# Performance work log

Hardware: AMD Instinct MI355X
Metric: run time of the kernel (lower is better)

Reference implementation:

```python
import jax, jax.numpy as jnp
import numpy as np


def _rel_coords_log(ws: int) -> np.ndarray:
    # matches torch.meshgrid default indexing='ij'
    idx = np.arange(ws, dtype=np.float32)
    coords = np.stack(np.meshgrid(idx, idx, indexing='ij'), axis=0).reshape(2, -1)  # [2, ws^2]
    rel = coords[:, :, None] - coords[:, None, :]  # [2, T, T]
    rel = rel.transpose(1, 2, 0).reshape(-1, 2)    # [T*T, 2]
    return np.sign(rel) * np.log1p(np.abs(rel))


def setup_inputs() -> dict:
    key = jax.random.key(0)
    ks = jax.random.split(key, 9)
    B, C, Hd, ws, meta_h = 256, 256, 8, 16, 256
    s = 1.0 / np.sqrt(C)
    return {
        'x': jax.random.normal(ks[0], (B, C, ws, ws), dtype=jnp.float32),
        'w_qkv': jax.random.normal(ks[1], (3 * C, C), dtype=jnp.float32) * s,
        'b_qkv': jax.random.normal(ks[2], (3 * C,), dtype=jnp.float32) * 0.01,
        'w_proj': jax.random.normal(ks[3], (C, C), dtype=jnp.float32) * s,
        'b_proj': jax.random.normal(ks[4], (C,), dtype=jnp.float32) * 0.01,
        'mw1': jax.random.normal(ks[5], (meta_h, 2), dtype=jnp.float32) * 0.5,
        'mb1': jax.random.normal(ks[6], (meta_h,), dtype=jnp.float32) * 0.01,
        'mw2': jax.random.normal(ks[7], (Hd, meta_h), dtype=jnp.float32) * (1.0 / np.sqrt(meta_h)),
        'mb2': jax.random.normal(ks[8], (Hd,), dtype=jnp.float32) * 0.01,
        'tau': jnp.ones((1, Hd, 1, 1), dtype=jnp.float32),
    }


def reference(x, w_qkv, b_qkv, w_proj, b_proj, mw1, mb1, mw2, mb2, tau):
    B, C, H, W = x.shape
    T = H * W
    nh = tau.shape[1]
    hd = C // nh
    # [B, C, H, W] -> [B, T, C]
    xt = x.reshape(B, C, T).transpose(0, 2, 1)
    qkv = xt @ w_qkv.T + b_qkv                                  # [B, T, 3C]
    qkv = qkv.reshape(B, T, 3, nh, hd).transpose(2, 0, 3, 1, 4)  # [3, B, nh, T, hd]
    q, k, v = qkv[0], qkv[1], qkv[2]
    # cosine similarity attention
    qn = jnp.linalg.norm(q, axis=-1, keepdims=True)              # [B, nh, T, 1]
    kn = jnp.linalg.norm(k, axis=-1, keepdims=True)
    denom = jnp.maximum(qn * kn.transpose(0, 1, 3, 2), 1e-6)
    scores = jnp.einsum('bhqd,bhkd->bhqk', q, k) / denom
    scores = scores / jnp.maximum(tau, 0.01)
    # MLP relative position bias (static coords)
    rc = jnp.asarray(_rel_coords_log(H))                          # [T*T, 2]
    bias = jax.nn.relu(rc @ mw1.T + mb1) @ mw2.T + mb2            # [T*T, nh]
    bias = bias.T.reshape(nh, T, T)
    scores = scores + bias[None]
    attn = jax.nn.softmax(scores, axis=-1)
    out = jnp.einsum('bhqk,bhkd->bhqd', attn, v)                  # [B, nh, T, hd]
    out = out.transpose(0, 2, 1, 3).reshape(B, T, C)
    out = out @ w_proj.T + b_proj
    return out.transpose(0, 2, 1).reshape(B, C, H, W)
```

## Files before the change

### kernel.cpp

```cpp
#include <hip/hip_runtime.h>
#include <math.h>

#define Cc 256
#define NH 8
#define HD 32
#define Tt 256
#define MH 256
#define TBL 961

typedef _Float16 f16;
typedef f16 f16x4 __attribute__((ext_vector_type(4)));
typedef f16 f16x8 __attribute__((ext_vector_type(8)));
typedef float f32x4 __attribute__((ext_vector_type(4)));

__device__ __forceinline__ f16x8 ld8(const f16* base, int row, int kc) {
  return *(const f16x8*)&base[row * 32 + ((kc ^ ((row >> 2) & 3)) << 3)];
}
__device__ __forceinline__ void st8(f16* base, int row, int kc, f16x8 v) {
  *(f16x8*)&base[row * 32 + ((kc ^ ((row >> 2) & 3)) << 3)] = v;
}
__device__ __forceinline__ int sidx(int row, int col) {
  return row * 32 + (((col >> 3) ^ ((row >> 2) & 3)) << 3) + (col & 7);
}
__device__ __forceinline__ int vsidx(int d, int t) {
  return d * 256 + (((t >> 3) ^ (d & 7)) << 3) + (t & 7);
}
__device__ __forceinline__ f16x8 vld8(const f16* base, int d, int tch) {
  return *(const f16x8*)&base[d * 256 + ((tch ^ (d & 7)) << 3)];
}

__global__ __launch_bounds__(256) void stage0_kernel(
    const float* __restrict__ x, f16* __restrict__ xt,
    const float* __restrict__ mw1, const float* __restrict__ mb1,
    const float* __restrict__ mw2, const float* __restrict__ mb2,
    const float* __restrict__ w_proj, const float* __restrict__ w_qkv,
    float* __restrict__ table, float* __restrict__ tablemax,
    f16* __restrict__ wpf, f16* __restrict__ wqf) {
  __shared__ __align__(16) char smem0[9216];
  int tid = threadIdx.x;
  int blk = blockIdx.x;

  if (blk < 4096) {
    f16* tile = (f16*)smem0;
    int b = blk >> 4, ti = (blk >> 2) & 3, tj = blk & 3;
    const float* xb = x + (size_t)b * 65536;
    int t4 = (tid & 15) * 4, cg = tid >> 4;
#pragma unroll
    for (int p = 0; p < 4; p++) {
      int cl = cg + p * 16;
      float4 v = *(const float4*)&xb[(size_t)(ti * 64 + cl) * 256 + tj * 64 + t4];
      const float* vp = (const float*)&v;
#pragma unroll
      for (int u = 0; u < 4; u++) {
        int tl = t4 + u;
        tile[tl * 72 + (((cl >> 3) ^ ((tl >> 2) & 7)) << 3) + (cl & 7)] = (f16)vp[u];
      }
    }
    __syncthreads();
    f16* xtb = xt + (size_t)b * 65536;
    int tr = tid >> 3, ck = tid & 7;
#pragma unroll
    for (int u = 0; u < 2; u++) {
      int r = tr + u * 32;
      f16x8 v = *(const f16x8*)&tile[r * 72 + ((ck ^ ((r >> 2) & 7)) << 3)];
      *(f16x8*)&xtb[(size_t)(tj * 64 + r) * 256 + ti * 64 + ck * 8] = v;
    }
    return;
  }

  blk -= 4096;
  if (blk >= NH + 32) {
    int blk2 = blk - NH - 32;
#pragma unroll
    for (int pass = 0; pass < 4; pass++) {
      int chunkid = blk2 * 256 + tid + pass * 6144;
      int row = chunkid >> 5, ck = chunkid & 31;
      int hh = row / 96, n = row % 96;
      int srow = ((n >> 5) << 8) + (hh << 5) + (n & 31);
      const float* wp = w_qkv + (size_t)srow * Cc + ck * 8;
      f16x8 v;
#pragma unroll
      for (int u = 0; u < 8; u++) v[u] = (f16)wp[u];
      *(f16x8*)&wqf[(size_t)row * Cc + ck * 8] = v;
    }
    return;
  }
  if (blk >= NH) {
    int base = (blk - NH) * 2048 + tid * 8;
    f16x8 v;
#pragma unroll
    for (int u = 0; u < 8; u++) v[u] = (f16)w_proj[base + u];
    *(f16x8*)&wpf[base] = v;
    return;
  }
  float4* s_w = (float4*)smem0;
  float* red = (float*)(smem0 + 4096);
  for (int i = tid; i < MH; i += 256) {
    float4 w;
    w.x = mw1[2 * i];
    w.y = mw1[2 * i + 1];
    w.z = mb1[i];
    w.w = mw2[blk * MH + i];
    s_w[i] = w;
  }
  __syncthreads();
  float b2 = mb2[blk];
  float d0v[4], d1v[4], ov[4];
#pragma unroll
  for (int j = 0; j < 4; j++) {
    int idx = tid + j * 256;
    int ii = idx < TBL ? idx : TBL - 1;
    float fdi = (float)(ii / 31 - 15);
    float fdj = (float)(ii % 31 - 15);
    d0v[j] = (fdi > 0.f ? 1.f : (fdi < 0.f ? -1.f : 0.f)) * log1pf(fabsf(fdi));
    d1v[j] = (fdj > 0.f ? 1.f : (fdj < 0.f ? -1.f : 0.f)) * log1pf(fabsf(fdj));
    ov[j] = b2;
  }
  for (int m = 0; m < MH; m++) {
    float4 w = s_w[m];
#pragma unroll
    for (int j = 0; j < 4; j++) {
      float hid = fmaxf(fmaf(d0v[j], w.x, fmaf(d1v[j], w.y, w.z)), 0.f);
      ov[j] = fmaf(hid, w.w, ov[j]);
    }
  }
  float lmax = -1e30f;
#pragma unroll
  for (int j = 0; j < 4; j++) {
    int idx = tid + j * 256;
    if (idx < TBL) {
      table[blk * TBL + idx] = ov[j];
      lmax = fmaxf(lmax, ov[j]);
    }
  }
  red[tid] = lmax;
  __syncthreads();
  for (int s = 128; s > 0; s >>= 1) {
    if (tid < s) red[tid] = fmaxf(red[tid], red[tid + s]);
    __syncthreads();
  }
  if (tid == 0) tablemax[blk] = red[0];
}

__global__ __launch_bounds__(512, 4) void fused_attn(
    const f16* __restrict__ xt, const f16* __restrict__ wqf,
    const float* __restrict__ b_qkv, const float* __restrict__ table,
    const float* __restrict__ tablemax, const float* __restrict__ tau,
    f16* __restrict__ attnH) {
  __shared__ __align__(16) char smem[67328];
  f16* Qa = (f16*)smem;
  f16* Ka = (f16*)(smem + 16384);
  f16* Vt = (f16*)(smem + 32768);
  f16* Pspare = (f16*)(smem + 49152);
  float* tbv = (float*)(smem + 51456);
  f16* Xa = (f16*)smem;
  f16* Wa = (f16*)(smem + 16384);

  int tid = threadIdx.x;
  int o = blockIdx.x;
  int bh = ((o & 7) << 8) | (o >> 3);
  int b = bh >> 3, h = bh & 7;
  int wv = tid >> 6, ln = tid & 63, lq = ln >> 4, lm = ln & 15;

  const float LOG2E = 1.4426950408889634f;
  float rtau = 1.0f / fmaxf(tau[h], 0.01f);
  float tmaxh = tablemax[h];

  for (int idx = tid; idx < 31 * 32; idx += 512) {
    int di_ = idx >> 5, c = idx & 31;
    float4 v;
    float* vp = (float*)&v;
#pragma unroll
    for (int u = 0; u < 4; u++) {
      int dj = c - u;
      dj = dj < 0 ? 0 : (dj > 30 ? 30 : dj);
      vp[u] = (table[h * TBL + di_ * 31 + dj] - tmaxh - rtau * 1.0001f) * LOG2E;
    }
    *(float4*)&tbv[idx * 4] = v;
  }

  float bj[6];
#pragma unroll
  for (int nt = 0; nt < 6; nt++) {
    int n = nt * 16 + lm;
    int row = ((n >> 5) << 8) + (h << 5) + (n & 31);
    bj[nt] = b_qkv[row];
  }

  const f16* xtb = xt + (size_t)b * 65536;
  const f16* wqh = wqf + (size_t)h * 24576;
  int xt_ = tid >> 1, xkc = (tid & 1) * 2;
  int wn = tid >> 2, wck = tid & 3;

  f32x4 acc[2][6] = {};
  f16x8 xv0, xv1, wvv;
  xv0 = *(const f16x8*)&xtb[xt_ * 256 + xkc * 8];
  xv1 = *(const f16x8*)&xtb[xt_ * 256 + xkc * 8 + 8];
  if (tid < 384) wvv = *(const f16x8*)&wqh[wn * 256 + wck * 8];

  for (int c0 = 0; c0 < Cc; c0 += 32) {
    st8(Xa, xt_, xkc, xv0);
    st8(Xa, xt_, xkc + 1, xv1);
    if (tid < 384) st8(Wa, wn, wck, wvv);
    __syncthreads();
    if (c0 + 32 < Cc) {
      xv0 = *(const f16x8*)&xtb[xt_ * 256 + c0 + 32 + xkc * 8];
      xv1 = *(const f16x8*)&xtb[xt_ * 256 + c0 + 32 + xkc * 8 + 8];
      if (tid < 384) wvv = *(const f16x8*)&wqh[wn * 256 + c0 + 32 + wck * 8];
    }
    f16x8 af[2], bf[6];
#pragma unroll
    for (int e = 0; e < 2; e++) af[e] = ld8(Xa, wv * 32 + e * 16 + lm, lq);
#pragma unroll
    for (int nt = 0; nt < 6; nt++) bf[nt] = ld8(Wa, nt * 16 + lm, lq);
#pragma unroll
    for (int e = 0; e < 2; e++)
#pragma unroll
      for (int nt = 0; nt < 6; nt++)
        acc[e][nt] = __builtin_amdgcn_mfma_f32_16x16x32_f16(af[e], bf[nt],
                                                            acc[e][nt], 0, 0, 0);
    __syncthreads();
  }

#pragma unroll
  for (int e = 0; e < 2; e++) {
#pragma unroll
    for (int nt = 0; nt < 6; nt++) {
      int d = (nt & 1) * 16 + lm;
      if (nt < 4) {
#pragma unroll
        for (int r = 0; r < 4; r++) {
          int t = wv * 32 + e * 16 + lq * 4 + r;
          f16 v = (f16)(acc[e][nt][r] + bj[nt]);
          if (nt < 2) Qa[sidx(t, d)] = v;
          else        Ka[sidx(t, d)] = v;
        }
      } else {
        int t0 = wv * 32 + e * 16 + lq * 4;
        f16x4 pv;
#pragma unroll
        for (int r = 0; r < 4; r++) pv[r] = (f16)(acc[e][nt][r] + bj[nt]);
        *(f16x4*)&Vt[vsidx(d, t0)] = pv;
      }
    }
  }
  __syncthreads();

  if (tid < 256) {
    int t = tid;
    float s = 0.f;
    f16x8 v[4];
#pragma unroll
    for (int ck = 0; ck < 4; ck++) {
      v[ck] = ld8(Qa, t, ck);
#pragma unroll
      for (int u = 0; u < 8; u++) { float f = (float)v[ck][u]; s = fmaf(f, f, s); }
    }
    float sc_ = rsqrtf(s) * rtau * LOG2E;
#pragma unroll
    for (int ck = 0; ck < 4; ck++) {
      f16x8 o2;
#pragma unroll
      for (int u = 0; u < 8; u++) o2[u] = (f16)((float)v[ck][u] * sc_);
      st8(Qa, t, ck, o2);
    }
  } else {
    int t = tid - 256;
    float s = 0.f;
    f16x8 v[4];
#pragma unroll
    for (int ck = 0; ck < 4; ck++) {
      v[ck] = ld8(Ka, t, ck);
#pragma unroll
      for (int u = 0; u < 8; u++) { float f = (float)v[ck][u]; s = fmaf(f, f, s); }
    }
    float sc_ = rsqrtf(s);
#pragma unroll
    for (int ck = 0; ck < 4; ck++) {
      f16x8 o2;
#pragma unroll
      for (int u = 0; u < 8; u++) o2[u] = (f16)((float)v[ck][u] * sc_);
      st8(Ka, t, ck, o2);
    }
  }
  __syncthreads();

  f16x8 qf[2];
#pragma unroll
  for (int e = 0; e < 2; e++) qf[e] = ld8(Qa, wv * 32 + e * 16 + lm, lq);
  __syncthreads();

  f16* Pme = (wv < 7) ? (Qa + wv * 1152) : Pspare;
  int c0l = lm - lq * 4 + 15;
  const float4* tbp = (const float4*)tbv;
  f32x4 acco[2][2] = {};
  f32x4 acco_s[2] = {};
  f16x8 onev;
#pragma unroll
  for (int u = 0; u < 8; u++) onev[u] = (f16)1.0f;
  int dibase = wv * 2 + 15;

  for (int n0 = 0; n0 < Tt; n0 += 32) {
    f16x8 kf[2];
#pragma unroll
    for (int nt = 0; nt < 2; nt++) kf[nt] = ld8(Ka, n0 + nt * 16 + lm, lq);
    f32x4 zero = {0.f, 0.f, 0.f, 0.f};
    f32x4 sc[2][2];
    __builtin_amdgcn_s_setprio(1);
#pragma unroll
    for (int e = 0; e < 2; e++)
#pragma unroll
      for (int nt = 0; nt < 2; nt++)
        sc[e][nt] = __builtin_amdgcn_mfma_f32_16x16x32_f16(kf[nt], qf[e], zero,
                                                           0, 0, 0);
    __builtin_amdgcn_s_setprio(0);
#pragma unroll
    for (int e = 0; e < 2; e++) {
#pragma unroll
      for (int nt = 0; nt < 2; nt++) {
        int di_ = dibase + e - (n0 >> 4) - nt;
        float4 bv = tbp[di_ * 32 + c0l];
        const float* bvp = (const float*)&bv;
        f16x4 pv;
#pragma unroll
        for (int r = 0; r < 4; r++) pv[r] = (f16)exp2f(sc[e][nt][r] + bvp[r]);
        *(f16x4*)&Pme[(e * 16 + lm) * 36 + nt * 16 + lq * 4] = pv;
      }
    }
    asm volatile("s_waitcnt lgkmcnt(0)" ::: "memory");
    f16x8 pf[2], vf[2];
#pragma unroll
    for (int e = 0; e < 2; e++) {
      f16x4 p0 = *(f16x4*)&Pme[(e * 16 + lm) * 36 + lq * 8];
      f16x4 p1 = *(f16x4*)&Pme[(e * 16 + lm) * 36 + lq * 8 + 4];
      pf[e] = __builtin_shufflevector(p0, p1, 0, 1, 2, 3, 4, 5, 6, 7);
    }
#pragma unroll
    for (int dt = 0; dt < 2; dt++)
      vf[dt] = vld8(Vt, dt * 16 + lm, (n0 >> 3) + lq);
    __builtin_amdgcn_s_setprio(1);
#pragma unroll
    for (int e = 0; e < 2; e++) {
#pragma unroll
      for (int dt = 0; dt < 2; dt++)
        acco[e][dt] = __builtin_amdgcn_mfma_f32_16x16x32_f16(pf[e], vf[dt],
                                                             acco[e][dt], 0, 0, 0);
      acco_s[e] = __builtin_amdgcn_mfma_f32_16x16x32_f16(pf[e], onev,
                                                         acco_s[e], 0, 0, 0);
    }
    __builtin_amdgcn_s_setprio(0);
  }

#pragma unroll
  for (int e = 0; e < 2; e++)
#pragma unroll
    for (int r = 0; r < 4; r++) {
      float rl = __builtin_amdgcn_rcpf(acco_s[e][r]);
      int q = wv * 32 + e * 16 + lq * 4 + r;
#pragma unroll
      for (int dt = 0; dt < 2; dt++) {
        int d = dt * 16 + lm;
        attnH[((size_t)b * Tt + q) * Cc + h * HD + d] =
            (f16)(acco[e][dt][r] * rl);
      }
    }
}

__global__ __launch_bounds__(256, 4) void proj_gemm(
    const f16* __restrict__ A, const f16* __restrict__ wf,
    const float* __restrict__ bp, float* __restrict__ out) {
  __shared__ __align__(16) f16 Af[128 * 72];
  __shared__ __align__(16) f16 Wsh[128 * 72];
  __shared__ float sB[128];
  int tid = threadIdx.x;
  int row0 = blockIdx.x * 128;
  int n0g = blockIdx.y * 128;
  int b = row0 >> 8, t0 = row0 & 255;
  int wv = tid >> 6, ln = tid & 63, lq = ln >> 4, lm = ln & 15;
  int cw = (wv & 1) * 64, tw = (wv >> 1) * 64;

  if (tid < 128) sB[tid] = bp[n0g + tid];

  f32x4 acc[4][4] = {};
  for (int k0 = 0; k0 < Cc; k0 += 64) {
#pragma unroll
    for (int p = 0; p < 4; p++) {
      int idx = p * 256 + tid;
      int row = idx >> 3, ch = idx & 7;
      f16x8 v = *(const f16x8*)&A[(size_t)(row0 + row) * Cc + k0 + ch * 8];
      *(f16x8*)&Af[row * 72 + ch * 8] = v;
    }
#pragma unroll
    for (int p = 0; p < 4; p++) {
      int idx = p * 256 + tid;
      int row = idx >> 3, ch = idx & 7;
      f16x8 v = *(const f16x8*)&wf[(size_t)(n0g + row) * Cc + k0 + ch * 8];
      *(f16x8*)&Wsh[row * 72 + ch * 8] = v;
    }
    __syncthreads();
#pragma unroll
    for (int kk = 0; kk < 2; kk++) {
      f16x8 wfr[4], af[4];
#pragma unroll
      for (int i = 0; i < 4; i++)
        wfr[i] = *(f16x8*)&Wsh[(cw + i * 16 + lm) * 72 + (kk * 4 + lq) * 8];
#pragma unroll
      for (int j = 0; j < 4; j++)
        af[j] = *(f16x8*)&Af[(tw + j * 16 + lm) * 72 + (kk * 4 + lq) * 8];
#pragma unroll
      for (int i = 0; i < 4; i++)
#pragma unroll
        for (int j = 0; j < 4; j++)
          acc[i][j] = __builtin_amdgcn_mfma_f32_16x16x32_f16(wfr[i], af[j],
                                                             acc[i][j], 0, 0, 0);
    }
    __syncthreads();
  }

#pragma unroll
  for (int i = 0; i < 4; i++)
#pragma unroll
    for (int r = 0; r < 4; r++) {
      int crl = cw + i * 16 + lq * 4 + r;
      float bias = sB[crl];
#pragma unroll
      for (int j = 0; j < 4; j++) {
        int tcl = tw + j * 16 + lm;
        out[(size_t)b * 65536 + (size_t)(n0g + crl) * 256 + t0 + tcl] =
            acc[i][j][r] + bias;
      }
    }
}

extern "C" void kernel_launch(void* const* d_in, const int* in_sizes, int n_in,
                              void* d_out, int out_size, void* d_ws,
                              size_t ws_size, hipStream_t stream) {
  const float* x = (const float*)d_in[0];
  const float* w_qkv = (const float*)d_in[1];
  const float* b_qkv = (const float*)d_in[2];
  const float* w_proj = (const float*)d_in[3];
  const float* b_proj = (const float*)d_in[4];
  const float* mw1 = (const float*)d_in[5];
  const float* mb1 = (const float*)d_in[6];
  const float* mw2 = (const float*)d_in[7];
  const float* mb2 = (const float*)d_in[8];
  const float* tau = (const float*)d_in[9];
  float* out = (float*)d_out;

  const size_t NEEDED = (size_t)(TBL * NH + NH) * 4 + (size_t)65536 * 2 +
                        (size_t)256 * NH * Tt * HD * 2;
  if (ws_size < NEEDED) return;

  float* table = (float*)d_ws;
  float* tablemax = table + TBL * NH;
  f16* wpf = (f16*)(tablemax + NH);
  f16* attnH = wpf + 65536;

  f16* xt = (f16*)d_out;
  f16* wqf = (f16*)d_out + (size_t)256 * 65536;

  stage0_kernel<<<4160, 256, 0, stream>>>(x, xt, mw1, mb1, mw2, mb2, w_proj,
                                          w_qkv, table, tablemax, wpf, wqf);
  fused_attn<<<256 * NH, 512, 0, stream>>>(xt, wqf, b_qkv, table, tablemax,
                                           tau, attnH);
  dim3 g3(512, 2);
  proj_gemm<<<g3, 256, 0, stream>>>(attnH, wpf, b_proj, out);
}
```

Before: 242.6 us.

## Software-pipeline attention loop: compute next QK scores during current PV MFMA

Peels the first QK^T tile out of the loop, then inside each iteration issues the next tile's K loads and score MFMAs before the current PV MFMAs and does the exp/bias write to the P buffer afterward. The aim is to overlap the exp2/bias VALU work and LDS traffic with matrix-core work and drop the explicit lgkmcnt wait. In exchange it raises register pressure from live score accumulators. It also relies on compiler barriers for ordering of the per-wave P buffer reuse, which is a potential LDS hazard.

```diff
diff --git a/kernel.cpp b/kernel.cpp
--- a/kernel.cpp
+++ b/kernel.cpp
@@ -299,12 +299,12 @@
 #pragma unroll
   for (int u = 0; u < 8; u++) onev[u] = (f16)1.0f;
   int dibase = wv * 2 + 15;
-
-  for (int n0 = 0; n0 < Tt; n0 += 32) {
+  f32x4 zero = {0.f, 0.f, 0.f, 0.f};
+
+  {
     f16x8 kf[2];
 #pragma unroll
-    for (int nt = 0; nt < 2; nt++) kf[nt] = ld8(Ka, n0 + nt * 16 + lm, lq);
-    f32x4 zero = {0.f, 0.f, 0.f, 0.f};
+    for (int nt = 0; nt < 2; nt++) kf[nt] = ld8(Ka, nt * 16 + lm, lq);
     f32x4 sc[2][2];
     __builtin_amdgcn_s_setprio(1);
 #pragma unroll
@@ -315,10 +315,10 @@
                                                            0, 0, 0);
     __builtin_amdgcn_s_setprio(0);
 #pragma unroll
-    for (int e = 0; e < 2; e++) {
+    for (int e = 0; e < 2; e++)
 #pragma unroll
       for (int nt = 0; nt < 2; nt++) {
-        int di_ = dibase + e - (n0 >> 4) - nt;
+        int di_ = dibase + e - nt;
         float4 bv = tbp[di_ * 32 + c0l];
         const float* bvp = (const float*)&bv;
         f16x4 pv;
@@ -326,8 +326,25 @@
         for (int r = 0; r < 4; r++) pv[r] = (f16)exp2f(sc[e][nt][r] + bvp[r]);
         *(f16x4*)&Pme[(e * 16 + lm) * 36 + nt * 16 + lq * 4] = pv;
       }
-    }
-    asm volatile("s_waitcnt lgkmcnt(0)" ::: "memory");
+    asm volatile("" ::: "memory");
+  }
+
+  for (int n0 = 0; n0 < Tt; n0 += 32) {
+    int nn = n0 + 32;
+    f32x4 sc[2][2];
+    if (nn < Tt) {
+      f16x8 kf[2];
+#pragma unroll
+      for (int nt = 0; nt < 2; nt++) kf[nt] = ld8(Ka, nn + nt * 16 + lm, lq);
+      __builtin_amdgcn_s_setprio(1);
+#pragma unroll
+      for (int e = 0; e < 2; e++)
+#pragma unroll
+        for (int nt = 0; nt < 2; nt++)
+          sc[e][nt] = __builtin_amdgcn_mfma_f32_16x16x32_f16(kf[nt], qf[e],
+                                                             zero, 0, 0, 0);
+      __builtin_amdgcn_s_setprio(0);
+    }
     f16x8 pf[2], vf[2];
 #pragma unroll
     for (int e = 0; e < 2; e++) {
@@ -338,6 +355,7 @@
 #pragma unroll
     for (int dt = 0; dt < 2; dt++)
       vf[dt] = vld8(Vt, dt * 16 + lm, (n0 >> 3) + lq);
+    asm volatile("" ::: "memory");
     __builtin_amdgcn_s_setprio(1);
 #pragma unroll
     for (int e = 0; e < 2; e++) {
@@ -349,6 +367,21 @@
                                                          acco_s[e], 0, 0, 0);
     }
     __builtin_amdgcn_s_setprio(0);
+    if (nn < Tt) {
+#pragma unroll
+      for (int e = 0; e < 2; e++)
+#pragma unroll
+        for (int nt = 0; nt < 2; nt++) {
+          int di_ = dibase + e - (nn >> 4) - nt;
+          float4 bv = tbp[di_ * 32 + c0l];
+          const float* bvp = (const float*)&bv;
+          f16x4 pv;
+#pragma unroll
+          for (int r = 0; r < 4; r++) pv[r] = (f16)exp2f(sc[e][nt][r] + bvp[r]);
+          *(f16x4*)&Pme[(e * 16 + lm) * 36 + nt * 16 + lq * 4] = pv;
+        }
+      asm volatile("" ::: "memory");
+    }
   }
 
 #pragma unroll
```

After: 240.7 us. Within noise of the previous version (-0.8%).
